# Kernel tuning notes

Measured on AMD Instinct MI355X. Metric: run time of the kernel, lower is better.

## Reference

```python
import jax, jax.numpy as jnp
import numpy as np
from jax import lax

ALPHA = 2.0        # elastic_alpha per axis
SMOOTH_NUM = 4
WIN = 5            # box smoothing window
FS = 11            # elastic field size per dim
SIZE_O = (128, 128, 128)


def _rodrigues(rot):
    # rot: (N,3) angle-axis -> (N,3,3) rotation matrix, with Taylor fallback near 0
    eps = 1e-6
    theta2 = jnp.sum(rot * rot, axis=1, keepdims=True)            # (N,1)
    theta = jnp.sqrt(jnp.maximum(theta2, eps))                    # safe sqrt
    w = rot / (theta + eps)
    wx, wy, wz = w[:, 0:1], w[:, 1:2], w[:, 2:3]
    c = jnp.cos(theta)
    s = jnp.sin(theta)
    k = 1.0 - c
    Rn = jnp.concatenate([
        c + wx * wx * k, wx * wy * k - wz * s, wy * s + wx * wz * k,
        wz * s + wx * wy * k, c + wy * wy * k, -wx * s + wy * wz * k,
        -wy * s + wx * wz * k, wx * s + wy * wz * k, c + wz * wz * k,
    ], axis=1).reshape(-1, 3, 3)
    rx, ry, rz = rot[:, 0:1], rot[:, 1:2], rot[:, 2:3]
    one = jnp.ones_like(rx)
    Rt = jnp.concatenate([one, -rz, ry, rz, one, -rx, -ry, rx, one],
                         axis=1).reshape(-1, 3, 3)
    mask = (theta2 > eps)[:, :, None]                             # (N,1,1)
    return jnp.where(mask, Rn, Rt)


def _box_smooth(d):
    # replicate-pad + mean box filter (torch __smooth_3d__)
    p = WIN // 2
    dp = jnp.pad(d, ((0, 0), (0, 0), (p, p), (p, p), (p, p)), mode='edge')
    k = jnp.ones((1, 1, WIN, WIN, WIN), d.dtype) / float(WIN ** 3)
    return lax.conv_general_dilated(dp, k, (1, 1, 1), 'VALID',
                                    dimension_numbers=('NCDHW', 'OIDHW', 'NCDHW'))


def _resize1d(x, axis, out_size):
    # linear interpolation along one axis, align_corners=False (torch interpolate)
    in_size = x.shape[axis]
    src = (jnp.arange(out_size, dtype=x.dtype) + 0.5) * (in_size / out_size) - 0.5
    src = jnp.clip(src, 0.0, in_size - 1.0)
    i0 = jnp.floor(src).astype(jnp.int32)
    i1 = jnp.minimum(i0 + 1, in_size - 1)
    w = (src - i0.astype(x.dtype))
    shape = [1] * x.ndim
    shape[axis] = out_size
    w = w.reshape(shape)
    x0 = jnp.take(x, i0, axis=axis)
    x1 = jnp.take(x, i1, axis=axis)
    return x0 * (1.0 - w) + x1 * w


def _resize3d(d, size):
    d = _resize1d(d, 2, size[0])
    d = _resize1d(d, 3, size[1])
    d = _resize1d(d, 4, size[2])
    return d


def _grid_sample3d(vol, grid):
    # vol: (N,C,D,H,W), grid: (N,D,H,W,3) normalized (x,y,z); trilinear, zeros pad,
    # align_corners=False (torch grid_sample defaults)
    N, C, D, H, W = vol.shape
    x = ((grid[..., 0] + 1.0) * W - 1.0) * 0.5
    y = ((grid[..., 1] + 1.0) * H - 1.0) * 0.5
    z = ((grid[..., 2] + 1.0) * D - 1.0) * 0.5
    x0f, y0f, z0f = jnp.floor(x), jnp.floor(y), jnp.floor(z)
    wx, wy, wz = x - x0f, y - y0f, z - z0f
    x0 = x0f.astype(jnp.int32)
    y0 = y0f.astype(jnp.int32)
    z0 = z0f.astype(jnp.int32)
    b = jnp.arange(N)[:, None, None, None]

    def gather(zi, yi, xi):
        valid = (zi >= 0) & (zi < D) & (yi >= 0) & (yi < H) & (xi >= 0) & (xi < W)
        v = vol[b, :, jnp.clip(zi, 0, D - 1), jnp.clip(yi, 0, H - 1),
                jnp.clip(xi, 0, W - 1)]                           # (N,Do,Ho,Wo,C)
        return v * valid[..., None].astype(vol.dtype)

    out = (gather(z0, y0, x0) * ((1 - wz) * (1 - wy) * (1 - wx))[..., None]
           + gather(z0, y0, x0 + 1) * ((1 - wz) * (1 - wy) * wx)[..., None]
           + gather(z0, y0 + 1, x0) * ((1 - wz) * wy * (1 - wx))[..., None]
           + gather(z0, y0 + 1, x0 + 1) * ((1 - wz) * wy * wx)[..., None]
           + gather(z0 + 1, y0, x0) * (wz * (1 - wy) * (1 - wx))[..., None]
           + gather(z0 + 1, y0, x0 + 1) * (wz * (1 - wy) * wx)[..., None]
           + gather(z0 + 1, y0 + 1, x0) * (wz * wy * (1 - wx))[..., None]
           + gather(z0 + 1, y0 + 1, x0 + 1) * (wz * wy * wx)[..., None])
    return jnp.transpose(out, (0, 4, 1, 2, 3))


def _field(raw, size):
    # raw uniform field -> scaled, smoothed, cropped, resized displacement (D,H,W)
    d = (raw - 0.5) * 2.0 * ALPHA
    for _ in range(SMOOTH_NUM):
        d = _box_smooth(d)
    p = WIN // 2
    d = d[:, :, p:p + FS, p:p + FS, p:p + FS]
    return _resize3d(d, size)[0, 0]


def _forward(vol, rot, scale, shift, dz, dy, dx):
    N, C, D, H, W = vol.shape
    R = _rodrigues(rot)                                  # (N,3,3)
    A = R * scale[:, None, :]                            # scale multiplies columns
    theta = jnp.concatenate([A, shift[:, :, None]], axis=2)  # (N,3,4)
    # base affine grid, align_corners=False: coord_i = (2i+1)/S - 1
    xs = (2.0 * jnp.arange(W, dtype=vol.dtype) + 1.0) / W - 1.0
    ys = (2.0 * jnp.arange(H, dtype=vol.dtype) + 1.0) / H - 1.0
    zs = (2.0 * jnp.arange(D, dtype=vol.dtype) + 1.0) / D - 1.0
    zz, yy, xx = jnp.meshgrid(zs, ys, xs, indexing='ij')
    pts = jnp.stack([xx, yy, zz, jnp.ones_like(xx)], axis=-1)    # (D,H,W,4)
    grid = jnp.einsum('nij,dhwj->ndhwi', theta, pts)             # (N,D,H,W,3)
    disp = jnp.stack([_field(dz, (D, H, W)), _field(dy, (D, H, W)),
                      _field(dx, (D, H, W))], axis=-1)           # (D,H,W,3)
    grid = grid + disp[None]
    out = _grid_sample3d(vol, grid)
    # central crop to SIZE_O
    zs0 = D // 2 - SIZE_O[0] // 2
    ys0 = H // 2 - SIZE_O[1] // 2
    xs0 = W // 2 - SIZE_O[2] // 2
    return out[:, :, zs0:zs0 + SIZE_O[0], ys0:ys0 + SIZE_O[1], xs0:xs0 + SIZE_O[2]]


def setup_inputs() -> dict:
    key = jax.random.key(0)
    k = jax.random.split(key, 7)
    vol = jax.random.normal(k[0], (4, 1, 160, 160, 160), dtype=jnp.float32)
    rot = (jax.random.uniform(k[1], (4, 3), dtype=jnp.float32) - 0.5) * 0.35   # ~±10 deg in rad
    scale = 0.9 + 0.2 * jax.random.uniform(k[2], (4, 3), dtype=jnp.float32)
    shift = (jax.random.uniform(k[3], (4, 3), dtype=jnp.float32) - 0.5) * 0.1
    dz = jax.random.uniform(k[4], (1, 1, 15, 15, 15), dtype=jnp.float32)
    dy = jax.random.uniform(k[5], (1, 1, 15, 15, 15), dtype=jnp.float32)
    dx = jax.random.uniform(k[6], (1, 1, 15, 15, 15), dtype=jnp.float32)
    return {"vol": vol, "rot": rot, "scale": scale, "shift": shift,
            "dz": dz, "dy": dy, "dx": dx}


def reference(vol, rot, scale, shift, dz, dy, dx):
    return _forward(vol, rot, scale, shift, dz, dy, dx)
```

## Files before the change

kernel.cpp:

```cpp
#include <hip/hip_runtime.h>

#define VD 160
#define OD 128
#define CROP0 16
#define FSZ 11
#define RAWSZ 15
#define NBATCH 4
#define ODQ 4

#define ESTR 17
#define E_CST (32*ESTR)

struct M15 { float v[15][15]; };
constexpr M15 mkB() {
    M15 b{};
    for (int i = 0; i < 15; ++i)
        for (int j = 0; j < 15; ++j) b.v[i][j] = 0.0f;
    for (int i = 0; i < 15; ++i)
        for (int t = -2; t <= 2; ++t) {
            int j = i + t; j = j < 0 ? 0 : (j > 14 ? 14 : j);
            b.v[i][j] += 0.2f;
        }
    return b;
}
constexpr M15 mmul(const M15& a, const M15& b) {
    M15 c{};
    for (int i = 0; i < 15; ++i)
        for (int j = 0; j < 15; ++j) {
            float s = 0.0f;
            for (int k = 0; k < 15; ++k) s += a.v[i][k] * b.v[k][j];
            c.v[i][j] = s;
        }
    return c;
}
constexpr M15 B2 = mmul(mkB(), mkB());
constexpr M15 B4 = mmul(B2, B2);

__global__ __launch_bounds__(1024) void prep_kernel(
        const float* __restrict__ rot, const float* __restrict__ scale,
        const float* __restrict__ shift,
        const float* __restrict__ dz, const float* __restrict__ dy,
        const float* __restrict__ dx,
        float* __restrict__ theta, float* __restrict__ fields) {
    const int tid = threadIdx.x;
    const int chan = blockIdx.x;

    if (chan == 3) {
        int n = tid;
        if (n >= NBATCH) return;
        float rx = rot[n*3+0], ry = rot[n*3+1], rz = rot[n*3+2];
        float t2 = rx*rx + ry*ry + rz*rz;
        const float eps = 1e-6f;
        float th = sqrtf(fmaxf(t2, eps));
        float inv = 1.0f / (th + eps);
        float wx = rx*inv, wy = ry*inv, wz = rz*inv;
        float c = cosf(th), s = sinf(th), k = 1.0f - c;
        float R[9];
        if (t2 > eps) {
            R[0] = c + wx*wx*k;      R[1] = wx*wy*k - wz*s;  R[2] = wy*s + wx*wz*k;
            R[3] = wz*s + wx*wy*k;   R[4] = c + wy*wy*k;     R[5] = -wx*s + wy*wz*k;
            R[6] = -wy*s + wx*wz*k;  R[7] = wx*s + wy*wz*k;  R[8] = c + wz*wz*k;
        } else {
            R[0] = 1.0f; R[1] = -rz;  R[2] = ry;
            R[3] = rz;   R[4] = 1.0f; R[5] = -rx;
            R[6] = -ry;  R[7] = rx;   R[8] = 1.0f;
        }
        for (int i = 0; i < 3; ++i) {
            for (int j = 0; j < 3; ++j)
                theta[n*12 + i*4 + j] = R[i*3 + j] * scale[n*3 + j];
            theta[n*12 + i*4 + 3] = shift[n*3 + i];
        }
        return;
    }

    __shared__ float bufA[RAWSZ*RAWSZ*RAWSZ];
    __shared__ float bufB[RAWSZ*RAWSZ*FSZ];
    __shared__ float bufC[RAWSZ*FSZ*FSZ];
    const float* raw = (chan == 0) ? dz : (chan == 1) ? dy : dx;
    const int NTOT = RAWSZ*RAWSZ*RAWSZ;

    for (int i = tid; i < NTOT; i += 1024)
        bufA[i] = (raw[i] - 0.5f) * 4.0f;
    __syncthreads();

    for (int i = tid; i < RAWSZ*RAWSZ*FSZ; i += 1024) {
        const int zy = i / FSZ;
        const int xo = i % FSZ;
        const float* row = &bufA[zy * RAWSZ];
        const float* w = B4.v[xo + 2];
        float s = 0.0f;
        #pragma unroll
        for (int j = 0; j < RAWSZ; ++j) s += row[j] * w[j];
        bufB[i] = s;
    }
    __syncthreads();

    for (int i = tid; i < RAWSZ*FSZ*FSZ; i += 1024) {
        const int z  = i / (FSZ*FSZ);
        const int r  = i % (FSZ*FSZ);
        const int yo = r / FSZ;
        const int xo = r % FSZ;
        const float* base = &bufB[z * (RAWSZ*FSZ) + xo];
        const float* w = B4.v[yo + 2];
        float s = 0.0f;
        #pragma unroll
        for (int j = 0; j < RAWSZ; ++j) s += base[j * FSZ] * w[j];
        bufC[i] = s;
    }
    __syncthreads();

    for (int i = tid; i < FSZ*FSZ*FSZ; i += 1024) {
        const int zo = i / (FSZ*FSZ);
        const int r  = i % (FSZ*FSZ);
        const float* base = &bufC[r];
        const float* w = B4.v[zo + 2];
        float s = 0.0f;
        #pragma unroll
        for (int j = 0; j < RAWSZ; ++j) s += base[j * (FSZ*FSZ)] * w[j];
        fields[chan*FSZ*FSZ*FSZ + i] = s;
    }
}

__device__ __forceinline__ void resize_coord(int m, int& i0, int& i1, float& w) {
    float s = fmaf((float)m + 0.5f, (float)FSZ / (float)VD, -0.5f);
    s = fminf(fmaxf(s, 0.0f), (float)(FSZ - 1));
    float f = floorf(s);
    i0 = (int)f;
    i1 = min(i0 + 1, FSZ - 1);
    w = s - f;
}

__global__ __launch_bounds__(512, 4) void sample_kernel(
        const float* __restrict__ vol, const float* __restrict__ theta,
        const float* __restrict__ fields, float* __restrict__ out) {
    __shared__ float e[3*E_CST];

    const int tid  = threadIdx.x;
    const int lane = tid & 63;
    const int wv   = tid >> 6;
    const int oh_l = wv & 3;
    const int wd   = wv >> 2;

    const int ow   = (blockIdx.x << 6) | lane;
    const int oh   = (blockIdx.y << 2) | oh_l;
    const int odb  = (blockIdx.z & 15) << 3;
    const int n    = blockIdx.z >> 4;
    const int od0  = odb + (wd << 2);

    {
        const int xi = tid & 15;
        const int rb = tid >> 4;
        if (xi < FSZ) {
            const int od_l  = rb & 7;
            const int oh_l2 = rb >> 3;
            int zi0, zi1, yi0, yi1; float zw, yw;
            resize_coord(odb + od_l + CROP0, zi0, zi1, zw);
            resize_coord((blockIdx.y << 2) + oh_l2 + CROP0, yi0, yi1, yw);
            const float w00 = (1.0f-zw)*(1.0f-yw), w01 = (1.0f-zw)*yw;
            const float w10 = zw*(1.0f-yw),        w11 = zw*yw;
            const int o00 = zi0*121 + yi0*11 + xi, o01 = zi0*121 + yi1*11 + xi;
            const int o10 = zi1*121 + yi0*11 + xi, o11 = zi1*121 + yi1*11 + xi;
            #pragma unroll
            for (int c = 0; c < 3; ++c) {
                const float* f = fields + c * (FSZ*FSZ*FSZ);
                e[(c*32 + rb)*ESTR + xi] =
                    80.0f * (f[o00]*w00 + f[o01]*w01 + f[o10]*w10 + f[o11]*w11);
            }
        }
    }

    const int w_ = ow + CROP0;

    const float x = fmaf(2.0f * (float)w_ + 1.0f, 1.0f / (float)VD, -1.0f);
    const float y = fmaf(2.0f * (float)(oh + CROP0) + 1.0f, 1.0f / (float)VD, -1.0f);

    float s = fmaf((float)w_ + 0.5f, (float)FSZ / (float)VD, -0.5f);
    s = fminf(fmaxf(s, 0.0f), (float)(FSZ - 1));
    const float sf = floorf(s);
    const int   xi0 = (int)sf;
    const float xw  = s - sf;

    const float* th = theta + n*12;
    const float cx = fmaf(th[0]*x + th[1]*y + th[3], 80.0f, 79.5f);
    const float cy = fmaf(th[4]*x + th[5]*y + th[7], 80.0f, 79.5f);
    const float cz = fmaf(th[8]*x + th[9]*y + th[11], 80.0f, 79.5f);
    const float tz0 = th[2] * 80.0f, tz1 = th[6] * 80.0f, tz2 = th[10] * 80.0f;

    const float* v = vol + (size_t)n * (VD*VD*VD);

    const float* ebase = &e[(oh_l*8 + (wd << 2))*ESTR + xi0];

    const float zb = fmaf(2.0f * (float)(od0 + CROP0) + 1.0f,
                          1.0f / (float)VD, -1.0f);
    float* op = out + ((((size_t)n*OD + od0)*OD + oh)*OD + ow);

    __syncthreads();

    float e0[3][ODQ], e1[3][ODQ];
    #pragma unroll
    for (int c = 0; c < 3; ++c)
        #pragma unroll
        for (int k = 0; k < ODQ; ++k) {
            e0[c][k] = ebase[c*E_CST + k*ESTR    ];
            e1[c][k] = ebase[c*E_CST + k*ESTR + 1];
        }

    float fx[ODQ], fy[ODQ], fz[ODQ];
    int ix[ODQ], iy[ODQ], iz[ODQ];
    int inb = 1;
    #pragma unroll
    for (int k = 0; k < ODQ; ++k) {
        const float z = zb + (float)k * (2.0f / (float)VD);
        const float d80x = fmaf(e1[0][k] - e0[0][k], xw, e0[0][k]);
        const float d80y = fmaf(e1[1][k] - e0[1][k], xw, e0[1][k]);
        const float d80z = fmaf(e1[2][k] - e0[2][k], xw, e0[2][k]);
        const float xs = fmaf(tz0, z, cx) + d80x;
        const float ys = fmaf(tz1, z, cy) + d80y;
        const float zs = fmaf(tz2, z, cz) + d80z;
        const float x0f = floorf(xs), y0f = floorf(ys), z0f = floorf(zs);
        fx[k] = xs - x0f; fy[k] = ys - y0f; fz[k] = zs - z0f;
        ix[k] = (int)x0f; iy[k] = (int)y0f; iz[k] = (int)z0f;
        inb &= ((unsigned)ix[k] < (unsigned)(VD-1)) &
               ((unsigned)iy[k] < (unsigned)(VD-1)) &
               ((unsigned)iz[k] < (unsigned)(VD-1));
    }

    if (__all(inb)) {
        float2 p00[ODQ], p01[ODQ], p10[ODQ], p11[ODQ];
        #pragma unroll
        for (int k = 0; k < ODQ; ++k) {
            const int b00 = (iz[k]*VD + iy[k])*VD + ix[k];
            __builtin_memcpy(&p00[k], v + b00,            sizeof(float2));
            __builtin_memcpy(&p01[k], v + b00 + VD,       sizeof(float2));
            __builtin_memcpy(&p10[k], v + b00 + VD*VD,    sizeof(float2));
            __builtin_memcpy(&p11[k], v + b00 + VD*VD+VD, sizeof(float2));
        }
        __builtin_amdgcn_sched_barrier(0);
        #pragma unroll
        for (int k = 0; k < ODQ; ++k)
            asm volatile("" :: "v"(p00[k].x), "v"(p00[k].y),
                               "v"(p01[k].x), "v"(p01[k].y),
                               "v"(p10[k].x), "v"(p10[k].y),
                               "v"(p11[k].x), "v"(p11[k].y));
        #pragma unroll
        for (int k = 0; k < ODQ; ++k) {
            const float r00 = fmaf(fx[k], p00[k].y - p00[k].x, p00[k].x);
            const float r01 = fmaf(fx[k], p01[k].y - p01[k].x, p01[k].x);
            const float r10 = fmaf(fx[k], p10[k].y - p10[k].x, p10[k].x);
            const float r11 = fmaf(fx[k], p11[k].y - p11[k].x, p11[k].x);
            const float r0 = fmaf(fy[k], r01 - r00, r00);
            const float r1 = fmaf(fy[k], r11 - r10, r10);
            op[(size_t)k*OD*OD] = fmaf(fz[k], r1 - r0, r0);
        }
    } else {
        #pragma unroll
        for (int k = 0; k < ODQ; ++k) {
            const int ix1 = ix[k] + 1, iy1 = iy[k] + 1, iz1 = iz[k] + 1;

            const float WX0 = ((unsigned)ix[k] < (unsigned)VD) ? (1.0f - fx[k]) : 0.0f;
            const float WX1 = ((unsigned)ix1   < (unsigned)VD) ? fx[k]          : 0.0f;
            const float WY0 = ((unsigned)iy[k] < (unsigned)VD) ? (1.0f - fy[k]) : 0.0f;
            const float WY1 = ((unsigned)iy1   < (unsigned)VD) ? fy[k]          : 0.0f;
            const float WZ0 = ((unsigned)iz[k] < (unsigned)VD) ? (1.0f - fz[k]) : 0.0f;
            const float WZ1 = ((unsigned)iz1   < (unsigned)VD) ? fz[k]          : 0.0f;

            const int xc0 = min(max(ix[k], 0), VD-1), xc1 = min(max(ix1, 0), VD-1);
            const int yc0 = min(max(iy[k], 0), VD-1), yc1 = min(max(iy1, 0), VD-1);
            const int zc0 = min(max(iz[k], 0), VD-1), zc1 = min(max(iz1, 0), VD-1);

            const int base = min(xc0, VD-2);
            const bool hi0 = (xc0 != base);
            const bool hi1 = (xc1 != base);
            const float wA = (hi0 ? 0.0f : WX0) + (hi1 ? 0.0f : WX1);
            const float wB = (hi0 ? WX0 : 0.0f) + (hi1 ? WX1 : 0.0f);

            const int sA = zc0*(VD*VD), sB = zc1*(VD*VD);
            const int tA = yc0*VD + base, tB = yc1*VD + base;

            float2 p00, p01, p10, p11;
            __builtin_memcpy(&p00, v + sA + tA, sizeof(float2));
            __builtin_memcpy(&p01, v + sA + tB, sizeof(float2));
            __builtin_memcpy(&p10, v + sB + tA, sizeof(float2));
            __builtin_memcpy(&p11, v + sB + tB, sizeof(float2));

            const float r00 = p00.x*wA + p00.y*wB;
            const float r01 = p01.x*wA + p01.y*wB;
            const float r10 = p10.x*wA + p10.y*wB;
            const float r11 = p11.x*wA + p11.y*wB;
            op[(size_t)k*OD*OD] = (r00*WY0 + r01*WY1)*WZ0 + (r10*WY0 + r11*WY1)*WZ1;
        }
    }
}

extern "C" void kernel_launch(void* const* d_in, const int* in_sizes, int n_in,
                              void* d_out, int out_size, void* d_ws, size_t ws_size,
                              hipStream_t stream) {
    const float* vol   = (const float*)d_in[0];
    const float* rot   = (const float*)d_in[1];
    const float* scale = (const float*)d_in[2];
    const float* shift = (const float*)d_in[3];
    const float* dz    = (const float*)d_in[4];
    const float* dy    = (const float*)d_in[5];
    const float* dx    = (const float*)d_in[6];
    float* out = (float*)d_out;

    float* ws     = (float*)d_ws;
    float* theta  = ws;
    float* fields = ws + 48;

    prep_kernel<<<4, 1024, 0, stream>>>(rot, scale, shift, dz, dy, dx,
                                        theta, fields);
    dim3 grid(OD/64, OD/4, (OD/8)*NBATCH);
    sample_kernel<<<grid, 512, 0, stream>>>(vol, theta, fields, out);
}
```

Baseline: 139.2 us.

## Stage per-block volume slab in LDS via global_load_lds for trilinear gathers

Retiles each block to a 16x8x8 output cube and computes the block's bounding box of source voxels with a wave-shuffle reduction plus a shared-memory reduction. It then copies that slab from global memory into LDS with direct global-to-LDS loads, and does the trilinear gathers from LDS. The goal is to replace scattered, poorly coalesced global gathers with coalesced bulk loads and cheap LDS reads. In exchange it adds two extra barriers, a large shared allocation (~55KB) that lowers occupancy, redundant loads of halo voxels, and a fallback for blocks whose footprint does not fit.

```diff
diff --git a/kernel.cpp b/kernel.cpp
--- a/kernel.cpp
+++ b/kernel.cpp
@@ -6,10 +6,15 @@
 #define FSZ 11
 #define RAWSZ 15
 #define NBATCH 4
-#define ODQ 4
+#define ODQ 2
 
 #define ESTR 17
-#define E_CST (32*ESTR)
+#define E_CST (64*ESTR)
+
+#define XSTR 33
+#define PLS  576
+#define ZMAX 22
+#define SLABF (ZMAX*PLS)
 
 struct M15 { float v[15][15]; };
 constexpr M15 mkB() {
@@ -130,47 +135,61 @@
     w = s - f;
 }
 
-__global__ __launch_bounds__(512, 4) void sample_kernel(
+__global__ __launch_bounds__(512) void sample_kernel(
         const float* __restrict__ vol, const float* __restrict__ theta,
         const float* __restrict__ fields, float* __restrict__ out) {
     __shared__ float e[3*E_CST];
+    __shared__ float slab[SLABF];
+    __shared__ int   red[8][8];
 
     const int tid  = threadIdx.x;
     const int lane = tid & 63;
+    const int wl   = lane & 15;
+    const int hl   = lane >> 4;
     const int wv   = tid >> 6;
-    const int oh_l = wv & 3;
-    const int wd   = wv >> 2;
-
-    const int ow   = (blockIdx.x << 6) | lane;
-    const int oh   = (blockIdx.y << 2) | oh_l;
+    const int wh   = wv & 1;
+    const int wd   = wv >> 1;
+
+    const int ow   = (blockIdx.x << 4) | wl;
+    const int oh_l = (wh << 2) | hl;
+    const int oh   = (blockIdx.y << 3) | oh_l;
     const int odb  = (blockIdx.z & 15) << 3;
     const int n    = blockIdx.z >> 4;
-    const int od0  = odb + (wd << 2);
+    const int od0  = odb + (wd << 1);
 
     {
         const int xi = tid & 15;
         const int rb = tid >> 4;
         if (xi < FSZ) {
-            const int od_l  = rb & 7;
-            const int oh_l2 = rb >> 3;
-            int zi0, zi1, yi0, yi1; float zw, yw;
+            const int od_l = rb & 7;
+            const int oh0  = rb >> 3;
+            int zi0, zi1, yA0, yA1, yB0, yB1;
+            float zw, ywA, ywB;
             resize_coord(odb + od_l + CROP0, zi0, zi1, zw);
-            resize_coord((blockIdx.y << 2) + oh_l2 + CROP0, yi0, yi1, yw);
-            const float w00 = (1.0f-zw)*(1.0f-yw), w01 = (1.0f-zw)*yw;
-            const float w10 = zw*(1.0f-yw),        w11 = zw*yw;
-            const int o00 = zi0*121 + yi0*11 + xi, o01 = zi0*121 + yi1*11 + xi;
-            const int o10 = zi1*121 + yi0*11 + xi, o11 = zi1*121 + yi1*11 + xi;
+            const int hbase = (blockIdx.y << 3) + CROP0;
+            resize_coord(hbase + oh0,     yA0, yA1, ywA);
+            resize_coord(hbase + oh0 + 4, yB0, yB1, ywB);
+            const float wz0 = 1.0f - zw;
+            const float wA00 = wz0*(1.0f-ywA), wA01 = wz0*ywA;
+            const float wA10 = zw*(1.0f-ywA),  wA11 = zw*ywA;
+            const float wB00 = wz0*(1.0f-ywB), wB01 = wz0*ywB;
+            const float wB10 = zw*(1.0f-ywB),  wB11 = zw*ywB;
+            const int oA00 = zi0*121 + yA0*11 + xi, oA01 = zi0*121 + yA1*11 + xi;
+            const int oA10 = zi1*121 + yA0*11 + xi, oA11 = zi1*121 + yA1*11 + xi;
+            const int oB00 = zi0*121 + yB0*11 + xi, oB01 = zi0*121 + yB1*11 + xi;
+            const int oB10 = zi1*121 + yB0*11 + xi, oB11 = zi1*121 + yB1*11 + xi;
             #pragma unroll
             for (int c = 0; c < 3; ++c) {
                 const float* f = fields + c * (FSZ*FSZ*FSZ);
-                e[(c*32 + rb)*ESTR + xi] =
-                    80.0f * (f[o00]*w00 + f[o01]*w01 + f[o10]*w10 + f[o11]*w11);
+                e[(c*64 + rb)*ESTR + xi] =
+                    80.0f * (f[oA00]*wA00 + f[oA01]*wA01 + f[oA10]*wA10 + f[oA11]*wA11);
+                e[(c*64 + rb + 32)*ESTR + xi] =
+                    80.0f * (f[oB00]*wB00 + f[oB01]*wB01 + f[oB10]*wB10 + f[oB11]*wB11);
             }
         }
     }
 
     const int w_ = ow + CROP0;
-
     const float x = fmaf(2.0f * (float)w_ + 1.0f, 1.0f / (float)VD, -1.0f);
     const float y = fmaf(2.0f * (float)(oh + CROP0) + 1.0f, 1.0f / (float)VD, -1.0f);
 
@@ -187,36 +206,25 @@
     const float tz0 = th[2] * 80.0f, tz1 = th[6] * 80.0f, tz2 = th[10] * 80.0f;
 
     const float* v = vol + (size_t)n * (VD*VD*VD);
-
-    const float* ebase = &e[(oh_l*8 + (wd << 2))*ESTR + xi0];
-
+    const float* ebase = &e[(oh_l*8 + (wd << 1))*ESTR + xi0];
     const float zb = fmaf(2.0f * (float)(od0 + CROP0) + 1.0f,
                           1.0f / (float)VD, -1.0f);
     float* op = out + ((((size_t)n*OD + od0)*OD + oh)*OD + ow);
 
     __syncthreads();
-
-    float e0[3][ODQ], e1[3][ODQ];
-    #pragma unroll
-    for (int c = 0; c < 3; ++c)
-        #pragma unroll
-        for (int k = 0; k < ODQ; ++k) {
-            e0[c][k] = ebase[c*E_CST + k*ESTR    ];
-            e1[c][k] = ebase[c*E_CST + k*ESTR + 1];
-        }
 
     float fx[ODQ], fy[ODQ], fz[ODQ];
     int ix[ODQ], iy[ODQ], iz[ODQ];
     int inb = 1;
     #pragma unroll
     for (int k = 0; k < ODQ; ++k) {
+        const float ex0 = ebase[        k*ESTR    ], ex1 = ebase[        k*ESTR + 1];
+        const float ey0 = ebase[E_CST + k*ESTR    ], ey1 = ebase[E_CST + k*ESTR + 1];
+        const float ez0 = ebase[2*E_CST + k*ESTR  ], ez1 = ebase[2*E_CST + k*ESTR + 1];
         const float z = zb + (float)k * (2.0f / (float)VD);
-        const float d80x = fmaf(e1[0][k] - e0[0][k], xw, e0[0][k]);
-        const float d80y = fmaf(e1[1][k] - e0[1][k], xw, e0[1][k]);
-        const float d80z = fmaf(e1[2][k] - e0[2][k], xw, e0[2][k]);
-        const float xs = fmaf(tz0, z, cx) + d80x;
-        const float ys = fmaf(tz1, z, cy) + d80y;
-        const float zs = fmaf(tz2, z, cz) + d80z;
+        const float xs = fmaf(tz0, z, cx) + fmaf(ex1 - ex0, xw, ex0);
+        const float ys = fmaf(tz1, z, cy) + fmaf(ey1 - ey0, xw, ey0);
+        const float zs = fmaf(tz2, z, cz) + fmaf(ez1 - ez0, xw, ez0);
         const float x0f = floorf(xs), y0f = floorf(ys), z0f = floorf(zs);
         fx[k] = xs - x0f; fy[k] = ys - y0f; fz[k] = zs - z0f;
         ix[k] = (int)x0f; iy[k] = (int)y0f; iz[k] = (int)z0f;
@@ -225,29 +233,67 @@
                ((unsigned)iz[k] < (unsigned)(VD-1));
     }
 
-    if (__all(inb)) {
-        float2 p00[ODQ], p01[ODQ], p10[ODQ], p11[ODQ];
+    const int BIG = 0x3fffffff;
+    int mnx = inb ? min(ix[0], ix[1]) : BIG,  mxx = inb ? max(ix[0], ix[1]) : -BIG;
+    int mny = inb ? min(iy[0], iy[1]) : BIG,  mxy = inb ? max(iy[0], iy[1]) : -BIG;
+    int mnz = inb ? min(iz[0], iz[1]) : BIG,  mxz = inb ? max(iz[0], iz[1]) : -BIG;
+    #pragma unroll
+    for (int d = 1; d < 64; d <<= 1) {
+        mnx = min(mnx, __shfl_xor(mnx, d));  mxx = max(mxx, __shfl_xor(mxx, d));
+        mny = min(mny, __shfl_xor(mny, d));  mxy = max(mxy, __shfl_xor(mxy, d));
+        mnz = min(mnz, __shfl_xor(mnz, d));  mxz = max(mxz, __shfl_xor(mxz, d));
+    }
+    if (lane == 0) {
+        red[wv][0] = mnx; red[wv][1] = mxx;
+        red[wv][2] = mny; red[wv][3] = mxy;
+        red[wv][4] = mnz; red[wv][5] = mxz;
+    }
+    __syncthreads();
+
+    int Mnx = BIG, Mxx = -BIG, Mny = BIG, Mxy = -BIG, Mnz = BIG, Mxz = -BIG;
+    #pragma unroll
+    for (int w2 = 0; w2 < 8; ++w2) {
+        Mnx = min(Mnx, red[w2][0]);  Mxx = max(Mxx, red[w2][1]);
+        Mny = min(Mny, red[w2][2]);  Mxy = max(Mxy, red[w2][3]);
+        Mnz = min(Mnz, red[w2][4]);  Mxz = max(Mxz, red[w2][5]);
+    }
+    const int lox = min(max(Mnx, 0), VD-2);
+    const int loy = min(max(Mny, 0), VD-2);
+    const int loz = min(max(Mnz, 0), VD-2);
+    const int XL = min(max(Mxx, 0), VD-2) - lox + 2;
+    const int YL = min(max(Mxy, 0), VD-2) - loy + 2;
+    const int ZL = min(max(Mxz, 0), VD-2) - loz + 2;
+    const bool fits = (Mnx <= Mxx) && (XL <= XSTR) && (YL <= 17) && (ZL <= ZMAX);
+
+    if (fits) {
+        const int NCH = ZL * 9;
+        for (int c = wv; c < NCH; c += 8) {
+            const int zc = c / 9;
+            const int r  = ((c - zc*9) << 6) + lane;
+            const int yy = r / XSTR;
+            const int xx = r - yy*XSTR;
+            int g = ((loz + zc)*VD + (loy + yy))*VD + (lox + xx);
+            g = min(g, VD*VD*VD - 1);
+            __builtin_amdgcn_global_load_lds(
+                (const __attribute__((address_space(1))) void*)(v + g),
+                (__attribute__((address_space(3))) void*)(slab + (c << 6) + lane),
+                4, 0, 0);
+        }
+    }
+    __syncthreads();
+
+    if (fits && __all(inb)) {
         #pragma unroll
         for (int k = 0; k < ODQ; ++k) {
-            const int b00 = (iz[k]*VD + iy[k])*VD + ix[k];
-            __builtin_memcpy(&p00[k], v + b00,            sizeof(float2));
-            __builtin_memcpy(&p01[k], v + b00 + VD,       sizeof(float2));
-            __builtin_memcpy(&p10[k], v + b00 + VD*VD,    sizeof(float2));
-            __builtin_memcpy(&p11[k], v + b00 + VD*VD+VD, sizeof(float2));
-        }
-        __builtin_amdgcn_sched_barrier(0);
-        #pragma unroll
-        for (int k = 0; k < ODQ; ++k)
-            asm volatile("" :: "v"(p00[k].x), "v"(p00[k].y),
-                               "v"(p01[k].x), "v"(p01[k].y),
-                               "v"(p10[k].x), "v"(p10[k].y),
-                               "v"(p11[k].x), "v"(p11[k].y));
-        #pragma unroll
-        for (int k = 0; k < ODQ; ++k) {
-            const float r00 = fmaf(fx[k], p00[k].y - p00[k].x, p00[k].x);
-            const float r01 = fmaf(fx[k], p01[k].y - p01[k].x, p01[k].x);
-            const float r10 = fmaf(fx[k], p10[k].y - p10[k].x, p10[k].x);
-            const float r11 = fmaf(fx[k], p11[k].y - p11[k].x, p11[k].x);
+            const float* sb = &slab[(iz[k]-loz)*PLS + (iy[k]-loy)*XSTR + (ix[k]-lox)];
+            const float a0 = sb[0],        a1 = sb[1];
+            const float a2 = sb[XSTR],     a3 = sb[XSTR+1];
+            const float b0 = sb[PLS],      b1 = sb[PLS+1];
+            const float b2 = sb[PLS+XSTR], b3 = sb[PLS+XSTR+1];
+            const float r00 = fmaf(fx[k], a1 - a0, a0);
+            const float r01 = fmaf(fx[k], a3 - a2, a2);
+            const float r10 = fmaf(fx[k], b1 - b0, b0);
+            const float r11 = fmaf(fx[k], b3 - b2, b2);
             const float r0 = fmaf(fy[k], r01 - r00, r00);
             const float r1 = fmaf(fy[k], r11 - r10, r10);
             op[(size_t)k*OD*OD] = fmaf(fz[k], r1 - r0, r0);
@@ -310,6 +356,6 @@
 
     prep_kernel<<<4, 1024, 0, stream>>>(rot, scale, shift, dz, dy, dx,
                                         theta, fields);
-    dim3 grid(OD/64, OD/4, (OD/8)*NBATCH);
+    dim3 grid(OD/16, OD/8, (OD/8)*NBATCH);
     sample_kernel<<<grid, 512, 0, stream>>>(vol, theta, fields, out);
 }
```

Measured after the change: 192.9 us. +38.5%, slower.
